# Kernel tuning notes

Hardware: AMD Instinct MI355X
Metric: run time of the kernel (lower is better)

The kernel has to match this reference:

```python
import jax, jax.numpy as jnp
import numpy as np

EPS = 1e-6

def _feature_map(x):
    # elu_feature_map: elu(x) + 1
    return jax.nn.elu(x) + 1.0

def setup_inputs() -> dict:
    key = jax.random.key(0)
    ks = jax.random.split(key, 7)
    B, C, H, W = 4, 128, 32, 32
    s = 1.0 / np.sqrt(C)
    return {
        "feature": jax.random.normal(ks[0], (B, C, H, W), dtype=jnp.float32),
        "wq": jax.random.normal(ks[1], (C, C), dtype=jnp.float32) * s,
        "bq": jax.random.normal(ks[2], (C,), dtype=jnp.float32) * s,
        "wk": jax.random.normal(ks[3], (C, C), dtype=jnp.float32) * s,
        "bk": jax.random.normal(ks[4], (C,), dtype=jnp.float32) * s,
        "wv": jax.random.normal(ks[5], (C, C), dtype=jnp.float32) * s,
        "bv": jax.random.normal(ks[6], (C,), dtype=jnp.float32) * s,
    }

def reference(feature, wq, bq, wk, bk, wv, bv):
    B, C, H, W = feature.shape
    # flatten(2).transpose(1,2): (B, C, H*W) -> (B, N, C)
    x = feature.reshape(B, C, H * W).transpose(0, 2, 1)
    # torch Linear: x @ W.T + b
    query = x @ wq.T + bq
    key_p = x @ wk.T + bk
    value = x @ wv.T + bv
    Q = _feature_map(query)  # (B, N, C)
    K = _feature_map(key_p)  # (B, N, C)
    # state=None path: Si = 0 + K; Ri = 0 + outer(K, V)
    Si = K                                           # (B, N, C)
    Ri = jnp.einsum('bnc,bnm->bncm', K, value)       # (B, N, C, M)
    Z = 1.0 / (jnp.einsum('bnc,bnc->bn', Q, Si) + EPS)  # (B, N)
    RLSA = jnp.einsum('bnc,bncm,bn->bnm', Q, Ri, Z)  # (B, N, M)
    return (RLSA, Ri, Si)
```

## Files before the change

### kernel.cpp

```cpp
#include <hip/hip_runtime.h>
#include <math.h>

#define C 128
#define N 1024
#define EPS 1e-6f

__global__ __launch_bounds__(128) void rlsa_kernel(
    const float* __restrict__ feat,
    const float* __restrict__ wq, const float* __restrict__ bq,
    const float* __restrict__ wk, const float* __restrict__ bk,
    const float* __restrict__ wv, const float* __restrict__ bv,
    float* __restrict__ out_rlsa, float* __restrict__ out_ri,
    float* __restrict__ out_si)
{
    __shared__ float xs[C];
    __shared__ float ks[C];
    __shared__ float vs[C];
    __shared__ float wsum[2];

    const int tid = threadIdx.x;
    const int bid = blockIdx.x;
    const int b = bid >> 10;
    const int n = bid & 1023;

    xs[tid] = feat[(size_t)b * C * N + (size_t)tid * N + n];
    __syncthreads();

    const float4* wq4 = (const float4*)(wq + tid * C);
    const float4* wk4 = (const float4*)(wk + tid * C);
    const float4* wv4 = (const float4*)(wv + tid * C);
    const float4* x4  = (const float4*)xs;
    float aq = 0.f, ak = 0.f, av = 0.f;
    #pragma unroll
    for (int j = 0; j < C / 4; ++j) {
        float4 xv = x4[j];
        float4 q = wq4[j];
        float4 k = wk4[j];
        float4 v = wv4[j];
        aq += xv.x * q.x + xv.y * q.y + xv.z * q.z + xv.w * q.w;
        ak += xv.x * k.x + xv.y * k.y + xv.z * k.z + xv.w * k.w;
        av += xv.x * v.x + xv.y * v.y + xv.z * v.z + xv.w * v.w;
    }
    aq += bq[tid];
    ak += bk[tid];
    av += bv[tid];

    float qf = aq > 0.f ? aq + 1.f : expf(aq);
    float kf = ak > 0.f ? ak + 1.f : expf(ak);
    float vf = av;

    ks[tid] = kf;
    vs[tid] = vf;

    float p = qf * kf;
    #pragma unroll
    for (int off = 32; off > 0; off >>= 1) p += __shfl_down(p, off, 64);
    if ((tid & 63) == 0) wsum[tid >> 6] = p;
    __syncthreads();
    const float S = wsum[0] + wsum[1];
    const float coef = S / (S + EPS);

    out_si[(size_t)bid * C + tid]   = kf;
    out_rlsa[(size_t)bid * C + tid] = coef * vf;

    float4* ri4 = (float4*)(out_ri + (size_t)bid * C * C);
    const float4* vs4 = (const float4*)vs;
    const int mq = tid & 31;
    const int chi = tid >> 5;
    #pragma unroll
    for (int i = 0; i < 32; ++i) {
        const float kc = ks[i * 4 + chi];
        float4 vv = vs4[mq];
        ri4[i * 128 + tid] = make_float4(kc * vv.x, kc * vv.y, kc * vv.z, kc * vv.w);
    }
}

extern "C" void kernel_launch(void* const* d_in, const int* in_sizes, int n_in,
                              void* d_out, int out_size, void* d_ws, size_t ws_size,
                              hipStream_t stream) {
    const float* feat = (const float*)d_in[0];
    const float* wq   = (const float*)d_in[1];
    const float* bq   = (const float*)d_in[2];
    const float* wk   = (const float*)d_in[3];
    const float* bk   = (const float*)d_in[4];
    const float* wv   = (const float*)d_in[5];
    const float* bv   = (const float*)d_in[6];

    float* out  = (float*)d_out;
    float* rlsa = out;
    float* ri   = out + (size_t)4 * 1024 * 128;
    float* si   = ri  + (size_t)4 * 1024 * 128 * 128;

    rlsa_kernel<<<4096, 128, 0, stream>>>(feat, wq, bq, wk, bk, wv, bv,
                                          rlsa, ri, si);
}
```

Baseline: 363.8 us.

## Split into tiled QKV projection kernel and separate outer-product write kernel

```diff
diff --git a/kernel.cpp b/kernel.cpp
--- a/kernel.cpp
+++ b/kernel.cpp
@@ -5,73 +5,132 @@
 #define N 1024
 #define EPS 1e-6f
 
-__global__ __launch_bounds__(128) void rlsa_kernel(
+#define TR 16
+#define XS_STRIDE 20
+
+__global__ __launch_bounds__(256) void qkv_kernel(
     const float* __restrict__ feat,
     const float* __restrict__ wq, const float* __restrict__ bq,
     const float* __restrict__ wk, const float* __restrict__ bk,
     const float* __restrict__ wv, const float* __restrict__ bv,
-    float* __restrict__ out_rlsa, float* __restrict__ out_ri,
-    float* __restrict__ out_si)
+    float* __restrict__ out_rlsa, float* __restrict__ out_si,
+    float* __restrict__ ws_v)
 {
-    __shared__ float xs[C];
-    __shared__ float ks[C];
-    __shared__ float vs[C];
-    __shared__ float wsum[2];
+    __shared__ float xs[C * XS_STRIDE];
+    __shared__ float sred[4][8];
 
-    const int tid = threadIdx.x;
-    const int bid = blockIdx.x;
-    const int b = bid >> 10;
-    const int n = bid & 1023;
+    const int t    = threadIdx.x;
+    const int c    = t & 127;
+    const int half = t >> 7;
+    const int row0 = blockIdx.x * TR;
+    const int b    = row0 >> 10;
+    const int n0   = row0 & 1023;
 
-    xs[tid] = feat[(size_t)b * C * N + (size_t)tid * N + n];
+    {
+        const float* fb = feat + (size_t)b * C * N;
+        #pragma unroll
+        for (int f = t; f < 512; f += 256) {
+            int j = f >> 2, q = f & 3;
+            float4 v = *(const float4*)(fb + (size_t)j * N + n0 + q * 4);
+            *(float4*)&xs[j * XS_STRIDE + q * 4] = v;
+        }
+    }
     __syncthreads();
 
-    const float4* wq4 = (const float4*)(wq + tid * C);
-    const float4* wk4 = (const float4*)(wk + tid * C);
-    const float4* wv4 = (const float4*)(wv + tid * C);
-    const float4* x4  = (const float4*)xs;
-    float aq = 0.f, ak = 0.f, av = 0.f;
+    float aq[8] = {0}, ak[8] = {0}, av[8] = {0};
+    const float4* wq4 = (const float4*)(wq + c * C);
+    const float4* wk4 = (const float4*)(wk + c * C);
+    const float4* wv4 = (const float4*)(wv + c * C);
+    const int xoff = half * 8;
+
+    #pragma unroll 8
+    for (int j4 = 0; j4 < 32; ++j4) {
+        float4 q4 = wq4[j4];
+        float4 k4 = wk4[j4];
+        float4 v4 = wv4[j4];
+        #pragma unroll
+        for (int u = 0; u < 4; ++u) {
+            const float* xr = &xs[(j4 * 4 + u) * XS_STRIDE + xoff];
+            float4 xa = *(const float4*)(xr);
+            float4 xb = *(const float4*)(xr + 4);
+            float wqv = (u == 0) ? q4.x : (u == 1) ? q4.y : (u == 2) ? q4.z : q4.w;
+            float wkv = (u == 0) ? k4.x : (u == 1) ? k4.y : (u == 2) ? k4.z : k4.w;
+            float wvv = (u == 0) ? v4.x : (u == 1) ? v4.y : (u == 2) ? v4.z : v4.w;
+            aq[0] += xa.x * wqv; aq[1] += xa.y * wqv; aq[2] += xa.z * wqv; aq[3] += xa.w * wqv;
+            aq[4] += xb.x * wqv; aq[5] += xb.y * wqv; aq[6] += xb.z * wqv; aq[7] += xb.w * wqv;
+            ak[0] += xa.x * wkv; ak[1] += xa.y * wkv; ak[2] += xa.z * wkv; ak[3] += xa.w * wkv;
+            ak[4] += xb.x * wkv; ak[5] += xb.y * wkv; ak[6] += xb.z * wkv; ak[7] += xb.w * wkv;
+            av[0] += xa.x * wvv; av[1] += xa.y * wvv; av[2] += xa.z * wvv; av[3] += xa.w * wvv;
+            av[4] += xb.x * wvv; av[5] += xb.y * wvv; av[6] += xb.z * wvv; av[7] += xb.w * wvv;
+        }
+    }
+
+    const float bqc = bq[c], bkc = bk[c], bvc = bv[c];
+    float qf[8], kf[8], vf[8];
     #pragma unroll
-    for (int j = 0; j < C / 4; ++j) {
-        float4 xv = x4[j];
-        float4 q = wq4[j];
-        float4 k = wk4[j];
-        float4 v = wv4[j];
-        aq += xv.x * q.x + xv.y * q.y + xv.z * q.z + xv.w * q.w;
-        ak += xv.x * k.x + xv.y * k.y + xv.z * k.z + xv.w * k.w;
-        av += xv.x * v.x + xv.y * v.y + xv.z * v.z + xv.w * v.w;
+    for (int i = 0; i < 8; ++i) {
+        float q = aq[i] + bqc;
+        float k = ak[i] + bkc;
+        qf[i] = q > 0.f ? q + 1.f : expf(q);
+        kf[i] = k > 0.f ? k + 1.f : expf(k);
+        vf[i] = av[i] + bvc;
     }
-    aq += bq[tid];
-    ak += bk[tid];
-    av += bv[tid];
 
-    float qf = aq > 0.f ? aq + 1.f : expf(aq);
-    float kf = ak > 0.f ? ak + 1.f : expf(ak);
-    float vf = av;
+    const int wave = t >> 6;
+    const int lane = t & 63;
+    #pragma unroll
+    for (int i = 0; i < 8; ++i) {
+        float p = qf[i] * kf[i];
+        #pragma unroll
+        for (int off = 32; off > 0; off >>= 1) p += __shfl_down(p, off, 64);
+        if (lane == 0) sred[wave][i] = p;
+    }
+    __syncthreads();
 
-    ks[tid] = kf;
-    vs[tid] = vf;
+    #pragma unroll
+    for (int i = 0; i < 8; ++i) {
+        float S = sred[half * 2][i] + sred[half * 2 + 1][i];
+        float coef = S / (S + EPS);
+        size_t ro = (size_t)(row0 + half * 8 + i) * C + c;
+        out_si[ro]   = kf[i];
+        out_rlsa[ro] = coef * vf[i];
+        ws_v[ro]     = vf[i];
+    }
+}
 
-    float p = qf * kf;
+#define BROWS 4
+
+__global__ __launch_bounds__(256) void ri_kernel(
+    const float* __restrict__ si, const float* __restrict__ ws_v,
+    float* __restrict__ out_ri)
+{
+    __shared__ float ks[BROWS * C];
+    __shared__ float vs[BROWS * C];
+
+    const int t  = threadIdx.x;
+    const int r0 = blockIdx.x * BROWS;
+
     #pragma unroll
-    for (int off = 32; off > 0; off >>= 1) p += __shfl_down(p, off, 64);
-    if ((tid & 63) == 0) wsum[tid >> 6] = p;
+    for (int idx = t; idx < BROWS * C; idx += 256) {
+        int rr = idx >> 7, cc = idx & 127;
+        ks[idx] = si[(size_t)(r0 + rr) * C + cc];
+        vs[idx] = ws_v[(size_t)(r0 + rr) * C + cc];
+    }
     __syncthreads();
-    const float S = wsum[0] + wsum[1];
-    const float coef = S / (S + EPS);
 
-    out_si[(size_t)bid * C + tid]   = kf;
-    out_rlsa[(size_t)bid * C + tid] = coef * vf;
-
-    float4* ri4 = (float4*)(out_ri + (size_t)bid * C * C);
     const float4* vs4 = (const float4*)vs;
-    const int mq = tid & 31;
-    const int chi = tid >> 5;
     #pragma unroll
-    for (int i = 0; i < 32; ++i) {
-        const float kc = ks[i * 4 + chi];
-        float4 vv = vs4[mq];
-        ri4[i * 128 + tid] = make_float4(kc * vv.x, kc * vv.y, kc * vv.z, kc * vv.w);
+    for (int rr = 0; rr < BROWS; ++rr) {
+        float4* ri4 = (float4*)(out_ri + (size_t)(r0 + rr) * C * C);
+        const float* krow = ks + rr * C;
+        const float4* vrow4 = vs4 + rr * 32;
+        #pragma unroll
+        for (int i = 0; i < 16; ++i) {
+            int f4 = i * 256 + t;
+            float kc = krow[f4 >> 5];
+            float4 vv = vrow4[f4 & 31];
+            ri4[f4] = make_float4(kc * vv.x, kc * vv.y, kc * vv.z, kc * vv.w);
+        }
     }
 }
 
@@ -91,6 +150,9 @@
     float* ri   = out + (size_t)4 * 1024 * 128;
     float* si   = ri  + (size_t)4 * 1024 * 128 * 128;
 
-    rlsa_kernel<<<4096, 128, 0, stream>>>(feat, wq, bq, wk, bk, wv, bv,
-                                          rlsa, ri, si);
+    float* ws_v = (float*)d_ws;
+
+    qkv_kernel<<<4096 / TR, 256, 0, stream>>>(feat, wq, bq, wk, bk, wv, bv,
+                                              rlsa, si, ws_v);
+    ri_kernel<<<4096 / BROWS, 256, 0, stream>>>(si, ws_v, ri);
 }
```

After: 296.2 us. 1.23x faster.
